# Kernel tuning notes

Hardware: AMD Instinct MI355X
Metric: run time of the kernel (lower is better)

Reference implementation:

```python
import jax, jax.numpy as jnp
import numpy as np
from jax import lax

B, V, C, H, W = 2, 8, 64, 128, 128
A = 256
C3 = 3 * C + 2  # 194 input channels for refine/confidence branches
CO = 3 * C      # 192 output channels of branch_refine
GROUPS = 8      # _group_count(192, 8) == 8
HID = max(4, CO // 4)  # 48 hidden channels in ChannelGate2d


def _conv3(x, w, b):
    y = lax.conv_general_dilated(x, w, (1, 1), 'SAME',
                                 dimension_numbers=('NCHW', 'OIHW', 'NCHW'))
    return y + b[None, :, None, None]


def _group_norm(x, scale, bias, groups, eps=1e-5):
    b, c, h, w = x.shape
    xg = x.reshape(b, groups, c // groups, h, w)
    mu = xg.mean(axis=(2, 3, 4), keepdims=True)
    var = xg.var(axis=(2, 3, 4), keepdims=True)
    xn = ((xg - mu) / jnp.sqrt(var + eps)).reshape(b, c, h, w)
    return xn * scale[None, :, None, None] + bias[None, :, None, None]


def _channel_gate(x, w1, b1, w2, b2):
    pooled = x.mean(axis=(2, 3))                     # [B,C]
    h = jax.nn.silu(pooled @ w1.T + b1)              # [B,HID]
    gate = jax.nn.sigmoid(h @ w2.T + b2)             # [B,C]
    return x * (0.5 + gate)[:, :, None, None]


def _conv_block(x, p):
    h = jax.nn.silu(_group_norm(_conv3(x, p['c1w'], p['c1b']), p['g1s'], p['g1b'], GROUPS))
    h = jax.nn.silu(_group_norm(_conv3(h, p['c2w'], p['c2b']), p['g2s'], p['g2b'], GROUPS))
    h = _channel_gate(h, p['gw1'], p['gb1'], p['gw2'], p['gb2'])
    res = jnp.einsum('bchw,oc->bohw', x, p['rpw']) + p['rpb'][None, :, None, None]
    return h + jnp.tanh(p['rs']) * res


def _fuse(vf, uvs, masks, importance, atlas_size):
    # vf:[B,V,C,H,W] uvs:[B,V,H,W,2] masks:[B,V,1,H,W] importance:[B,V]
    b, v, c, h, w = vf.shape
    P = atlas_size * atlas_size
    weights = jnp.maximum(importance.astype(vf.dtype), 0.0)
    finite = jnp.isfinite(uvs).all(axis=-1)                 # [B,V,H,W]
    valid = (masks[:, :, 0] > 0.5) & finite & (weights[:, :, None, None] > 0.0)
    safe = jnp.where(finite[..., None], uvs, 0.0)
    xi = jnp.round(jnp.clip(safe[..., 0], 0.0, 1.0) * (atlas_size - 1)).astype(jnp.int32)
    yi = jnp.round((1.0 - jnp.clip(safe[..., 1], 0.0, 1.0)) * (atlas_size - 1)).astype(jnp.int32)
    idx = (yi * atlas_size + xi).reshape(b, v * h * w)      # [B,N]
    wvalid = valid.astype(vf.dtype) * weights[:, :, None, None]
    feat = (vf * wvalid[:, :, None]).transpose(0, 2, 1, 3, 4).reshape(b, c, v * h * w)
    cnt = wvalid.reshape(b, v * h * w)

    def per_sample(f, cc, i):
        atlas = jax.ops.segment_sum(f.T, i, num_segments=P).T   # [C,P]
        counts = jax.ops.segment_sum(cc, i, num_segments=P)     # [P]
        return atlas, counts

    atlas, counts = jax.vmap(per_sample)(feat, cnt, idx)
    atlas = atlas.reshape(b, c, atlas_size, atlas_size)
    counts = counts.reshape(b, 1, atlas_size, atlas_size)
    fused = atlas / jnp.maximum(counts, 1.0)
    return fused, (counts > 0).astype(vf.dtype)


def _normalize_per_sample(t, eps=1e-6):
    scale = jnp.maximum(t.reshape(t.shape[0], -1).max(axis=1), eps)
    return jnp.clip(t / scale[:, None, None, None], 0.0, 1.0)


def setup_inputs() -> dict:
    key = jax.random.key(0)
    ks = jax.random.split(key, 20)
    inp = {
        'encoded_views': jax.random.normal(ks[0], (B, V, C, H, W), jnp.float32),
        'view_uvs': jax.random.uniform(ks[1], (B, V, H, W, 2), jnp.float32),
        'view_masks': jax.random.uniform(ks[2], (B, V, 1, H, W), jnp.float32),
        'w_global': jax.random.uniform(ks[3], (B, V), jnp.float32),
        'w_boundary': jax.random.uniform(ks[4], (B, V), jnp.float32),
        'w_highlight': jax.random.uniform(ks[5], (B, V), jnp.float32),
        'atlas_size': A,
        # ConvBlock params (random instead of zero-init so all paths are exercised)
        'c1w': jax.random.normal(ks[6], (CO, C3, 3, 3), jnp.float32) * 0.02,
        'c1b': jnp.zeros((CO,), jnp.float32),
        'g1s': jnp.ones((CO,), jnp.float32),
        'g1b': jnp.zeros((CO,), jnp.float32),
        'c2w': jax.random.normal(ks[7], (CO, CO, 3, 3), jnp.float32) * 0.02,
        'c2b': jnp.zeros((CO,), jnp.float32),
        'g2s': jnp.ones((CO,), jnp.float32),
        'g2b': jnp.zeros((CO,), jnp.float32),
        'gw1': jax.random.normal(ks[8], (HID, CO), jnp.float32) * 0.05,
        'gb1': jnp.zeros((HID,), jnp.float32),
        'gw2': jax.random.normal(ks[9], (CO, HID), jnp.float32) * 0.05,
        'gb2': jnp.zeros((CO,), jnp.float32),
        'rpw': jax.random.normal(ks[10], (CO, C3), jnp.float32) * 0.05,
        'rpb': jnp.zeros((CO,), jnp.float32),
        'rs': jnp.array(0.3, jnp.float32),
        'conf_w': jax.random.normal(ks[11], (3, C3), jnp.float32) * 0.05,
        'conf_b': jnp.zeros((3,), jnp.float32),
        'mix_scale': jnp.array(0.5, jnp.float32),
    }
    return inp


def reference(encoded_views, view_uvs, view_masks, w_global, w_boundary, w_highlight,
              atlas_size, c1w, c1b, g1s, g1b, c2w, c2b, g2s, g2b,
              gw1, gb1, gw2, gb2, rpw, rpb, rs, conf_w, conf_b, mix_scale):
    p = dict(c1w=c1w, c1b=c1b, g1s=g1s, g1b=g1b, c2w=c2w, c2b=c2b, g2s=g2s, g2b=g2b,
             gw1=gw1, gb1=gb1, gw2=gw2, gb2=gb2, rpw=rpw, rpb=rpb, rs=rs)
    g_feat, g_val = _fuse(encoded_views, view_uvs, view_masks, w_global, atlas_size)
    b_feat, b_val = _fuse(encoded_views, view_uvs, view_masks, w_boundary, atlas_size)
    h_feat, h_val = _fuse(encoded_views, view_uvs, view_masks, w_highlight, atlas_size)
    coverage = jnp.clip((g_val + b_val + h_val) / 3.0, 0.0, 1.0)
    stack = jnp.stack([g_feat, b_feat, h_feat], axis=1)     # [B,3,C,A,A]
    uncertainty = jnp.sqrt(stack.var(axis=1).mean(axis=1, keepdims=True))
    uncertainty = _normalize_per_sample(uncertainty) * coverage
    ctx = jnp.concatenate([g_feat, b_feat, h_feat, coverage, uncertainty], axis=1)
    refine = _conv_block(ctx, p)
    rg, rb, rh = jnp.split(refine, 3, axis=1)
    conf = jax.nn.sigmoid(jnp.einsum('bchw,oc->bohw', ctx, conf_w) + conf_b[None, :, None, None])
    ms = jnp.tanh(mix_scale)
    g_out = g_feat + ms * rg * conf[:, 0:1]
    b_out = b_feat + ms * rb * conf[:, 1:2]
    h_out = h_feat + ms * rh * conf[:, 2:3]
    return (g_out, b_out, h_out, coverage, uncertainty, conf)
```

## Files before the change

### kernel.cpp

```cpp
#include <hip/hip_runtime.h>
#include <math.h>

#define B_ 2
#define V_ 8
#define C_ 64
#define HW_ 16384
#define A_ 256
#define P_ 65536
#define CO_ 192
#define CPG_ 24
#define NG_ 8
#define ICP1 224
#define ICP2 192

#define OFF_ACC   0ull
#define SZ_ACC    (2ull*65536*192*4)
#define OFF_CNT   (OFF_ACC + SZ_ACC)
#define SZ_CNT    (2ull*3*65536*4)
#define OFF_CTXB  (OFF_CNT + SZ_CNT)
#define SZ_CTXB   (2ull*65536*224*2)
#define OFF_H1A   (OFF_CTXB + SZ_CTXB)
#define SZ_H1A    (2ull*65536*192*2)
#define OFF_W1    (OFF_H1A + SZ_H1A)
#define SZ_W1     (9ull*192*224*2)
#define OFF_W2    (OFF_W1 + SZ_W1)
#define SZ_W2     (9ull*192*192*2)
#define OFF_SM    (OFF_W2 + SZ_W2 + 256)

#define SM_STATS1 0
#define SM_STATS2 256
#define SM_SCALE  512
#define SM_POOLED 1024
#define SM_GATE   2560
#define SM_RAWU   8192

#define OUT_B    8388608
#define OUT_COV  25165824
#define OUT_UNC  25296896
#define OUT_CONF 25427968

typedef __attribute__((ext_vector_type(4))) float f32x4;
typedef __attribute__((ext_vector_type(8))) short bf16x8;

__device__ __forceinline__ float sigmoidf_(float x){ return 1.f/(1.f+expf(-x)); }
__device__ __forceinline__ float bf2f(unsigned short h){ return __uint_as_float(((unsigned)h)<<16); }
__device__ __forceinline__ unsigned short f2bf(float f){
  unsigned u = __float_as_uint(f);
  return (unsigned short)((u + 0x7fffu + ((u>>16)&1u)) >> 16);
}

__device__ __forceinline__ void gl_lds16(const void* g, void* l){
  __builtin_amdgcn_global_load_lds((const __attribute__((address_space(1))) void*)g,
                                   (__attribute__((address_space(3))) void*)l, 16, 0, 0);
}

__global__ __launch_bounds__(256) void k_prep(const float* __restrict__ c1w,
    const float* __restrict__ c2w, unsigned short* __restrict__ w1p, unsigned short* __restrict__ w2p)
{
  int idx = blockIdx.x*256 + threadIdx.x;
  const int N1 = 9*192*224;
  if (idx < N1){
    int ic = idx % 224; int oc = (idx/224) % 192; int k = idx/(224*192);
    float v = (ic < 194) ? c1w[(size_t)(oc*194+ic)*9 + k] : 0.f;
    w1p[idx] = f2bf(v);
  } else {
    int i2 = idx - N1;
    if (i2 < 9*192*192){
      int ic = i2 % 192; int oc = (i2/192) % 192; int k = i2/(192*192);
      w2p[i2] = f2bf(c2w[(size_t)(oc*192+ic)*9 + k]);
    }
  }
}

__global__ __launch_bounds__(256) void k_fuse(const float* __restrict__ vf,
    const float* __restrict__ uvs, const float* __restrict__ masks,
    const float* __restrict__ wgp, const float* __restrict__ wbp, const float* __restrict__ whp,
    float* __restrict__ acc, float* __restrict__ cnt)
{
  __shared__ __align__(16) float sf[64*65];
  __shared__ int sidx[64];
  __shared__ int svalid[64];
  __shared__ float sw[3];
  int t = threadIdx.x;
  int pix0 = blockIdx.x*64;
  int b   = pix0 / (V_*HW_);
  int rem = pix0 % (V_*HW_);
  int v   = rem / HW_;
  int p2  = rem % HW_;
  size_t vbase = ((size_t)(b*V_+v))*C_*HW_;
  for (int i=0;i<16;i++){
    int f = t + i*256;
    int c = f>>6, px = f&63;
    sf[c*65+px] = vf[vbase + (size_t)c*HW_ + p2 + px];
  }
  if (t<64){
    const float* u2 = uvs + (((size_t)(b*V_+v))*HW_ + p2 + t)*2;
    float ux = u2[0], uy = u2[1];
    int fin = isfinite(ux) && isfinite(uy);
    float su = fin?ux:0.f, svv = fin?uy:0.f;
    float cu = fminf(fmaxf(su,0.f),1.f);
    float cv = fminf(fmaxf(svv,0.f),1.f);
    int xi = (int)rintf(cu*255.f);
    int yi = (int)rintf((1.f-cv)*255.f);
    sidx[t] = yi*256+xi;
    float m = masks[((size_t)(b*V_+v))*HW_ + p2 + t];
    svalid[t] = (m>0.5f) && fin;
  }
  if (t<3){
    const float* wp = (t==0)?wgp:((t==1)?wbp:whp);
    sw[t] = fmaxf(wp[b*V_+v], 0.f);
  }
  __syncthreads();
  int wave = t>>6, lane = t&63;
  float w0 = sw[0], w1 = sw[1], w2 = sw[2];
  for (int i=0;i<16;i++){
    int px = wave*16+i;
    if (!svalid[px]) continue;
    int bin = sidx[px];
    float val = sf[lane*65+px];
    size_t base = ((size_t)b*P_ + bin)*192;
    if (w0>0.f) atomicAdd(&acc[base + lane],        val*w0);
    if (w1>0.f) atomicAdd(&acc[base + 64 + lane],   val*w1);
    if (w2>0.f) atomicAdd(&acc[base + 128 + lane],  val*w2);
    if (lane<3){
      float wv = sw[lane];
      if (wv>0.f) atomicAdd(&cnt[((size_t)(b*3+lane))*P_ + bin], wv);
    }
  }
}

__global__ __launch_bounds__(256) void k_finalize(const float* __restrict__ acc,
      const float* __restrict__ cnt, unsigned short* __restrict__ ctxb,
      float* __restrict__ out_cov, float* __restrict__ raw_unc, int* __restrict__ scale)
{
  __shared__ __align__(16) float sv[64*193];
  __shared__ float sc[3][64];
  __shared__ float up[256];
  __shared__ float s_cov[64];
  __shared__ float s_unc[64];
  int t = threadIdx.x;
  int bin0 = blockIdx.x*64;
  int b = bin0 >> 16;
  int p0 = bin0 & 65535;
  size_t abase = ((size_t)b*P_ + p0)*192;
  for (int i=0;i<48;i++){
    int f = t + i*256;
    int bl = f/192, c = f - bl*192;
    sv[bl*193+c] = acc[abase + f];
  }
  if (t<192){
    int br = t>>6, bl = t&63;
    sc[br][bl] = cnt[((size_t)(b*3+br))*P_ + p0 + bl];
  }
  __syncthreads();
  {
    int bl = t>>2, q = t&3;
    float dg = 1.f/fmaxf(sc[0][bl],1.f);
    float db = 1.f/fmaxf(sc[1][bl],1.f);
    float dh = 1.f/fmaxf(sc[2][bl],1.f);
    float s = 0.f;
    for (int j=0;j<16;j++){
      int c = q*16+j;
      float fg = sv[bl*193+c]*dg;
      float fb = sv[bl*193+64+c]*db;
      float fh = sv[bl*193+128+c]*dh;
      sv[bl*193+c]=fg; sv[bl*193+64+c]=fb; sv[bl*193+128+c]=fh;
      float m = (fg+fb+fh)*(1.f/3.f);
      float d0=fg-m, d1=fb-m, d2=fh-m;
      s += d0*d0+d1*d1+d2*d2;
    }
    up[t] = s;
  }
  __syncthreads();
  if (t<64){
    float tot = up[t*4]+up[t*4+1]+up[t*4+2]+up[t*4+3];
    float u = sqrtf(tot*(1.f/192.f));
    float vg = sc[0][t]>0.f?1.f:0.f;
    float vb = sc[1][t]>0.f?1.f:0.f;
    float vh = sc[2][t]>0.f?1.f:0.f;
    float cov = fminf(fmaxf((vg+vb+vh)*(1.f/3.f),0.f),1.f);
    s_cov[t] = cov; s_unc[t] = u;
    out_cov[(size_t)b*P_ + p0 + t] = cov;
    raw_unc[(size_t)b*P_ + p0 + t] = u;
    atomicMax(&scale[b], __float_as_int(u));
  }
  __syncthreads();
  for (int f=t; f<1792; f+=256){
    int cg = f % 28, bl = f / 28;
    int c0 = cg*8;
    unsigned short h[8];
    #pragma unroll
    for (int j=0;j<8;j++){
      int c = c0+j;
      float vv;
      if (c < 192)      vv = sv[bl*193+c];
      else if (c==192)  vv = s_cov[bl];
      else if (c==193)  vv = s_unc[bl];
      else              vv = 0.f;
      h[j] = f2bf(vv);
    }
    *(uint4*)&ctxb[((size_t)b*P_ + p0 + bl)*ICP1 + c0] = *(uint4*)h;
  }
}

__global__ __launch_bounds__(256) void k_norm_unc(unsigned short* __restrict__ ctxb,
    const int* __restrict__ scale, const float* __restrict__ raw_unc,
    const float* __restrict__ out_cov, float* __restrict__ out_unc)
{
  int tid = blockIdx.x*256 + threadIdx.x;
  int b = tid >> 16;
  float s = fmaxf(__int_as_float(scale[b]), 1e-6f);
  float u = raw_unc[tid];
  float cov = out_cov[tid];
  float un = fminf(fmaxf(u/s,0.f),1.f)*cov;
  out_unc[tid] = un;
  ctxb[(size_t)tid*ICP1 + 193] = f2bf(un);
}

template<int ICP, int CHUNKS>
__global__ __launch_bounds__(256,2) void k_conv3(const unsigned short* __restrict__ X,
    const unsigned short* __restrict__ Wp, const float* __restrict__ bias, float* __restrict__ Y,
    double* __restrict__ stats)
{
  __shared__ short s_in[2][258*32];
  __shared__ short s_w[576*32];
  __shared__ float sred[2][64];
  __shared__ float gsm[16];
  int t = threadIdx.x;
  int f_ = blockIdx.x + 128*(blockIdx.y + 3*blockIdx.z);
  int xcd = f_ & 7; int g_ = f_ >> 3;
  int ypair = xcd*16 + (g_ & 15);
  int h_  = g_ >> 4;
  int b   = h_ & 1;
  int oc0 = (h_ >> 1)*64;
  int y0  = ypair*2;
  int wv = t>>6, lane = t&63, l15 = lane&15, quad = lane>>4;

  f32x4 accA[4][4], accB[4][4];
  #pragma unroll
  for (int mt=0;mt<4;mt++){
    float4 bv = *(const float4*)&bias[oc0 + mt*16 + quad*4];
    f32x4 iv; iv.x=bv.x; iv.y=bv.y; iv.z=bv.z; iv.w=bv.w;
    #pragma unroll
    for (int nt=0;nt<4;nt++){ accA[mt][nt]=iv; accB[mt][nt]=iv; }
  }

  const unsigned short* Xb = X + (size_t)b*P_*ICP;

  if (t < 128){
    int bufi = t>>6, j = t&63;
    int idx = (j<32) ? j : (257*32 + (j-32));
    s_in[bufi][idx] = 0;
  }
  if (t < 128) sred[t>>6][t&63] = 0.f;
  if (t < 16)  gsm[t] = 0.f;

  auto issue_input = [&](int c2, int j2){
    int gy = y0 - 1 + j2;
    gy = min(max(gy,0),255);
    const unsigned short* src = Xb + ((size_t)gy*256)*ICP + c2*32;
    short* dst = &s_in[j2&1][0];
    #pragma unroll
    for (int i=0;i<4;i++){
      int f = t + i*256;
      int xi = 1 + (f>>2), icq = f&3;
      int icg = icq ^ ((xi>>1)&3);
      gl_lds16(src + (size_t)(xi-1)*ICP + icg*8, dst + 32 + (size_t)f*8);
    }
  };
  auto issue_wa = [&](int c2){
    int ic0n = c2*32;
    #pragma unroll
    for (int i=0;i<6;i++){
      int f = t + i*256;
      int oc = (f>>2)&63, icq = f&3;
      int r = i*64 + oc;
      int icg = icq ^ ((r>>1)&3);
      gl_lds16(Wp + ((size_t)(i*192) + oc0 + oc)*ICP + ic0n + icg*8, &s_w[(size_t)f*8]);
    }
  };
  auto issue_wb = [&](int c2){
    int ic0n = c2*32;
    #pragma unroll
    for (int i=0;i<3;i++){
      int f = t + i*256;
      int oc = (f>>2)&63, icq = f&3;
      int r = (6+i)*64 + oc;
      int icg = icq ^ ((r>>1)&3);
      gl_lds16(Wp + ((size_t)((6+i)*192) + oc0 + oc)*ICP + ic0n + icg*8, &s_w[(size_t)(1536+f)*8]);
    }
  };

  issue_wa(0);
  issue_input(0,0);
  issue_wb(0);
  issue_input(0,1);
  asm volatile("s_waitcnt lgkmcnt(0)" ::: "memory");

  for (int c=0; c<CHUNKS; ++c){
    #pragma unroll
    for (int j=0;j<4;++j){
      if (j==0)      asm volatile("s_waitcnt vmcnt(7)" ::: "memory");
      else if (j==1) asm volatile("s_waitcnt vmcnt(4)" ::: "memory");
      else if (j==2) asm volatile("s_waitcnt vmcnt(4)" ::: "memory");
      else {
        if (c==CHUNKS-1) asm volatile("s_waitcnt vmcnt(0)"  ::: "memory");
        else             asm volatile("s_waitcnt vmcnt(10)" ::: "memory");
      }
      __builtin_amdgcn_s_barrier();
      __builtin_amdgcn_sched_barrier(0);

      bool doA = (j<=2) && (y0 + j >= 1);
      bool doB = (j>=1) && (y0 - 1 + j <= 255);
      const short* si = &s_in[j&1][0];
      if (doA || doB){
        #pragma unroll
        for (int kx=0;kx<3;kx++){
          bf16x8 Bf[4];
          #pragma unroll
          for (int nt=0;nt<4;nt++){
            int r = wv*64 + nt*16 + l15 + kx;
            Bf[nt] = *(const bf16x8*)&si[r*32 + ((quad ^ ((r>>1)&3)))*8];
          }
          if (doA){
            bf16x8 Af[4];
            #pragma unroll
            for (int mt=0;mt<4;mt++){
              int r = j*192 + kx*64 + mt*16 + l15;
              Af[mt] = *(const bf16x8*)&s_w[r*32 + ((quad ^ ((r>>1)&3)))*8];
            }
            #pragma unroll
            for (int mt=0;mt<4;mt++)
              #pragma unroll
              for (int nt=0;nt<4;nt++)
                accA[mt][nt] = __builtin_amdgcn_mfma_f32_16x16x32_bf16(Af[mt], Bf[nt], accA[mt][nt], 0, 0, 0);
          }
          if (doB){
            bf16x8 Af[4];
            #pragma unroll
            for (int mt=0;mt<4;mt++){
              int r = (j-1)*192 + kx*64 + mt*16 + l15;
              Af[mt] = *(const bf16x8*)&s_w[r*32 + ((quad ^ ((r>>1)&3)))*8];
            }
            #pragma unroll
            for (int mt=0;mt<4;mt++)
              #pragma unroll
              for (int nt=0;nt<4;nt++)
                accB[mt][nt] = __builtin_amdgcn_mfma_f32_16x16x32_bf16(Af[mt], Bf[nt], accB[mt][nt], 0, 0, 0);
          }
        }
      }
      __builtin_amdgcn_s_barrier();
      __builtin_amdgcn_sched_barrier(0);
      if (j==2 && c+1<CHUNKS) issue_wa(c+1);
      if (j==3 && c+1<CHUNKS) issue_wb(c+1);
      if (!(c==CHUNKS-1 && j>=2))
        issue_input(j>=2 ? c+1 : c, (j+2)&3);
    }
  }

  float* Yb = Y + (size_t)b*P_*192;
  #pragma unroll
  for (int mt=0;mt<4;mt++){
    int oc = oc0 + mt*16 + quad*4;
    #pragma unroll
    for (int nt=0;nt<4;nt++){
      int px = wv*64 + nt*16 + l15;
      *(f32x4*)&Yb[(size_t)(y0*256+px)*192 + oc]     = accA[mt][nt];
      *(f32x4*)&Yb[(size_t)((y0+1)*256+px)*192 + oc] = accB[mt][nt];
    }
  }

  #pragma unroll
  for (int mt=0;mt<4;mt++)
    #pragma unroll
    for (int jj=0;jj<4;jj++){
      float v1 = accA[mt][0][jj]+accA[mt][1][jj]+accA[mt][2][jj]+accA[mt][3][jj]
               + accB[mt][0][jj]+accB[mt][1][jj]+accB[mt][2][jj]+accB[mt][3][jj];
      float v2 = accA[mt][0][jj]*accA[mt][0][jj]+accA[mt][1][jj]*accA[mt][1][jj]
               + accA[mt][2][jj]*accA[mt][2][jj]+accA[mt][3][jj]*accA[mt][3][jj]
               + accB[mt][0][jj]*accB[mt][0][jj]+accB[mt][1][jj]*accB[mt][1][jj]
               + accB[mt][2][jj]*accB[mt][2][jj]+accB[mt][3][jj]*accB[mt][3][jj];
      v1 += __shfl_xor(v1,1); v1 += __shfl_xor(v1,2); v1 += __shfl_xor(v1,4); v1 += __shfl_xor(v1,8);
      v2 += __shfl_xor(v2,1); v2 += __shfl_xor(v2,2); v2 += __shfl_xor(v2,4); v2 += __shfl_xor(v2,8);
      if (l15==0){
        int ocl = mt*16 + quad*4 + jj;
        atomicAdd(&sred[0][ocl], v1);
        atomicAdd(&sred[1][ocl], v2);
      }
    }
  __syncthreads();
  if (t < 64){
    int g = (oc0 + t)/24;
    atomicAdd(&gsm[g*2],   sred[0][t]);
    atomicAdd(&gsm[g*2+1], sred[1][t]);
  }
  __syncthreads();
  if (t < 8){
    int glo = oc0/24, ghi = (oc0+63)/24;
    if (t >= glo && t <= ghi){
      atomicAdd(&stats[(b*8+t)*2],   (double)gsm[t*2]);
      atomicAdd(&stats[(b*8+t)*2+1], (double)gsm[t*2+1]);
    }
  }
}

__global__ __launch_bounds__(256) void k_gn1_apply(const float* __restrict__ x, const double* __restrict__ stats,
    const float* __restrict__ gs, const float* __restrict__ gb, unsigned short* __restrict__ y)
{
  size_t i8 = ((size_t)blockIdx.x*256 + threadIdx.x)*8;
  int b = (int)(i8 / ((size_t)192*P_));
  int c = (int)(i8 % 192);
  int bg = b*8 + c/24;
  const double N = 24.0*65536.0;
  double mu = stats[bg*2]/N;
  double var = stats[bg*2+1]/N - mu*mu;
  float rstd = 1.0f/sqrtf((float)var + 1e-5f);
  float mean = (float)mu;
  float4 sA = *(const float4*)&gs[c];
  float4 sB = *(const float4*)&gs[c+4];
  float4 bA = *(const float4*)&gb[c];
  float4 bB = *(const float4*)&gb[c+4];
  float4 v0 = *(const float4*)&x[i8];
  float4 v1 = *(const float4*)&x[i8+4];
  float xin[8] = {v0.x,v0.y,v0.z,v0.w,v1.x,v1.y,v1.z,v1.w};
  float scl[8] = {sA.x,sA.y,sA.z,sA.w,sB.x,sB.y,sB.z,sB.w};
  float bia[8] = {bA.x,bA.y,bA.z,bA.w,bB.x,bB.y,bB.z,bB.w};
  unsigned short h[8];
  #pragma unroll
  for (int i=0;i<8;i++){
    float xn = (xin[i]-mean)*rstd*scl[i] + bia[i];
    h[i] = f2bf(xn*sigmoidf_(xn));
  }
  *(uint4*)&y[i8] = *(uint4*)h;
}

__global__ __launch_bounds__(256) void k_gn2_apply(float* __restrict__ x, const double* __restrict__ stats,
    const float* __restrict__ gs, const float* __restrict__ gb, float* __restrict__ pooled)
{
  __shared__ float pl[384];
  int t = threadIdx.x;
  for (int f=t; f<384; f+=256) pl[f]=0.f;
  int tid = blockIdx.x*256 + t;
  int c = (tid*8) % 192;
  float4 sA = *(const float4*)&gs[c];
  float4 sB = *(const float4*)&gs[c+4];
  float4 bA = *(const float4*)&gb[c];
  float4 bB = *(const float4*)&gb[c+4];
  float scl[8] = {sA.x,sA.y,sA.z,sA.w,sB.x,sB.y,sB.z,sB.w};
  float bia[8] = {bA.x,bA.y,bA.z,bA.w,bB.x,bB.y,bB.z,bB.w};
  float mean[2], rstd[2];
  #pragma unroll
  for (int bb=0;bb<2;bb++){
    int bg = bb*8 + c/24;
    const double N = 24.0*65536.0;
    double mu = stats[bg*2]/N;
    double var = stats[bg*2+1]/N - mu*mu;
    rstd[bb] = 1.0f/sqrtf((float)var + 1e-5f);
    mean[bb] = (float)mu;
  }
  float pacc[2][8] = {{0.f}};
  __syncthreads();
  #pragma unroll
  for (int k=0;k<8;k++){
    size_t i8 = ((size_t)tid + (size_t)k*393216)*8;
    int bb = k>>2;
    float4 v0 = *(const float4*)&x[i8];
    float4 v1 = *(const float4*)&x[i8+4];
    float xin[8] = {v0.x,v0.y,v0.z,v0.w,v1.x,v1.y,v1.z,v1.w};
    #pragma unroll
    for (int i=0;i<8;i++){
      float xn = (xin[i]-mean[bb])*rstd[bb]*scl[i] + bia[i];
      xn = xn*sigmoidf_(xn);
      xin[i] = xn;
      pacc[bb][i] += xn;
    }
    *(float4*)&x[i8]   = make_float4(xin[0],xin[1],xin[2],xin[3]);
    *(float4*)&x[i8+4] = make_float4(xin[4],xin[5],xin[6],xin[7]);
  }
  #pragma unroll
  for (int bb=0;bb<2;bb++)
    #pragma unroll
    for (int i=0;i<8;i++) atomicAdd(&pl[bb*192 + c + i], pacc[bb][i]);
  __syncthreads();
  for (int f=t; f<384; f+=256) atomicAdd(&pooled[f], pl[f]*(1.f/65536.f));
}

__global__ void k_gate(const float* __restrict__ pooled, const float* __restrict__ gw1,
    const float* __restrict__ gb1, const float* __restrict__ gw2, const float* __restrict__ gb2,
    float* __restrict__ gatef)
{
  __shared__ float hb[2*48];
  int t = threadIdx.x;
  if (t<96){
    int b=t/48, j=t%48;
    float a = gb1[j];
    for (int c=0;c<192;c++) a = fmaf(pooled[b*192+c], gw1[j*192+c], a);
    hb[t] = a*sigmoidf_(a);
  }
  __syncthreads();
  for (int i=t;i<384;i+=256){
    int b=i/192, c=i%192;
    float a = gb2[c];
    for (int j=0;j<48;j++) a = fmaf(hb[b*48+j], gw2[c*48+j], a);
    gatef[i] = 0.5f + sigmoidf_(a);
  }
}

__global__ __launch_bounds__(256) void k_conf(const unsigned short* __restrict__ ctxb,
    const float* __restrict__ cw, const float* __restrict__ cbias, float* __restrict__ out_conf)
{
  __shared__ float scw[3*224];
  int t = threadIdx.x;
  for (int f=t; f<672; f+=256){
    int c = f % 224, o = f / 224;
    scw[f] = (c<194) ? cw[o*194 + c] : 0.f;
  }
  __syncthreads();
  int tid = blockIdx.x*256 + t;
  int b = tid >> 16, p = tid & 65535;
  const unsigned short* cp = ctxb + ((size_t)b*P_ + p)*ICP1;
  float a0 = cbias[0], a1 = cbias[1], a2 = cbias[2];
  for (int q=0;q<28;q++){
    uint4 v = *(const uint4*)&cp[q*8];
    unsigned wd[4] = {v.x,v.y,v.z,v.w};
    #pragma unroll
    for (int j=0;j<8;j++){
      unsigned bits = wd[j>>1];
      float xf = (j&1) ? __uint_as_float(bits & 0xffff0000u) : __uint_as_float(bits<<16);
      int c = q*8+j;
      a0 = fmaf(xf, scw[c],       a0);
      a1 = fmaf(xf, scw[224+c],   a1);
      a2 = fmaf(xf, scw[448+c],   a2);
    }
  }
  out_conf[((size_t)(b*3+0))*P_ + p] = sigmoidf_(a0);
  out_conf[((size_t)(b*3+1))*P_ + p] = sigmoidf_(a1);
  out_conf[((size_t)(b*3+2))*P_ + p] = sigmoidf_(a2);
}

__global__ __launch_bounds__(256,4) void k_combine(const unsigned short* __restrict__ ctxb,
    const float* __restrict__ h2, const float* __restrict__ rpw, const float* __restrict__ rpb,
    const float* __restrict__ gatef, const float* __restrict__ conf_out,
    const float* __restrict__ rs, const float* __restrict__ mix, float* __restrict__ dout)
{
  __shared__ short s_x[256*32];
  __shared__ short s_w[64*32];
  int t = threadIdx.x;
  size_t p0 = (size_t)blockIdx.x*256;
  int oc0 = blockIdx.y*64, br = blockIdx.y;
  int wv = t>>6, lane = t&63, l15 = lane&15, quad = lane>>4;
  f32x4 acc[4][4];
  #pragma unroll
  for (int mt=0;mt<4;mt++){
    float4 bv = *(const float4*)&rpb[oc0 + mt*16 + quad*4];
    f32x4 iv; iv.x=bv.x; iv.y=bv.y; iv.z=bv.z; iv.w=bv.w;
    #pragma unroll
    for (int nt=0;nt<4;nt++) acc[mt][nt]=iv;
  }
  for (int ch=0; ch<7; ch++){
    int ic0 = ch*32;
    __syncthreads();
    for (int f=t; f<1024; f+=256){
      int icq = f&3, px = f>>2;
      uint4 v = *(const uint4*)&ctxb[(p0+px)*ICP1 + ic0 + icq*8];
      *(uint4*)&s_x[px*32 + ((icq ^ ((px>>1)&3)))*8] = v;
    }
    {
      int oc = t&63, icq = t>>6;
      unsigned short h[8];
      #pragma unroll
      for (int j=0;j<8;j++){
        int ic = ic0 + icq*8 + j;
        h[j] = (ic<194) ? f2bf(rpw[(size_t)(oc0+oc)*194 + ic]) : (unsigned short)0;
      }
      *(uint4*)&s_w[oc*32 + ((icq ^ ((oc>>1)&3)))*8] = *(uint4*)h;
    }
    __syncthreads();
    bf16x8 Af[4], Bf[4];
    #pragma unroll
    for (int mt=0;mt<4;mt++){
      int r = mt*16 + l15;
      Af[mt] = *(const bf16x8*)&s_w[r*32 + (((quad ^ ((r>>1)&3)))&3)*8];
    }
    #pragma unroll
    for (int nt=0;nt<4;nt++){
      int r = wv*64 + nt*16 + l15;
      Bf[nt] = *(const bf16x8*)&s_x[r*32 + (((quad ^ ((r>>1)&3)))&3)*8];
    }
    #pragma unroll
    for (int mt=0;mt<4;mt++)
      #pragma unroll
      for (int nt=0;nt<4;nt++)
        acc[mt][nt] = __builtin_amdgcn_mfma_f32_16x16x32_bf16(Af[mt], Bf[nt], acc[mt][nt], 0, 0, 0);
  }
  float trs = tanhf(rs[0]);
  float ms2 = tanhf(mix[0]);
  int b = (int)(p0 >> 16);
  #pragma unroll
  for (int mt=0;mt<4;mt++){
    int oc = oc0 + mt*16 + quad*4;
    int cc = oc & 63;
    float4 gv = *(const float4*)&gatef[b*192 + oc];
    #pragma unroll
    for (int nt=0;nt<4;nt++){
      size_t pf = p0 + wv*64 + nt*16 + l15;
      int p = (int)(pf & 65535);
      ushort4 fh = *(const ushort4*)&ctxb[pf*ICP1 + oc];
      float4 hv = *(const float4*)&h2[pf*192 + oc];
      float cf = conf_out[((size_t)(b*3+br))*P_ + p];
      size_t dst = (size_t)br*OUT_B + ((size_t)(b*64+cc))*P_ + p;
      dout[dst]            = bf2f(fh.x) + ms2*(hv.x*gv.x + trs*acc[mt][nt].x)*cf;
      dout[dst + P_]       = bf2f(fh.y) + ms2*(hv.y*gv.y + trs*acc[mt][nt].y)*cf;
      dout[dst + 2*P_]     = bf2f(fh.z) + ms2*(hv.z*gv.z + trs*acc[mt][nt].z)*cf;
      dout[dst + 3*P_]     = bf2f(fh.w) + ms2*(hv.w*gv.w + trs*acc[mt][nt].w)*cf;
    }
  }
}

extern "C" void kernel_launch(void* const* d_in, const int* in_sizes, int n_in,
                              void* d_out, int out_size, void* d_ws, size_t ws_size,
                              hipStream_t stream)
{
  const float* vf    = (const float*)d_in[0];
  const float* uvs   = (const float*)d_in[1];
  const float* masks = (const float*)d_in[2];
  const float* wg    = (const float*)d_in[3];
  const float* wb    = (const float*)d_in[4];
  const float* wh    = (const float*)d_in[5];
  const float* c1w = (const float*)d_in[7];
  const float* c1b = (const float*)d_in[8];
  const float* g1s = (const float*)d_in[9];
  const float* g1b = (const float*)d_in[10];
  const float* c2w = (const float*)d_in[11];
  const float* c2b = (const float*)d_in[12];
  const float* g2s = (const float*)d_in[13];
  const float* g2b = (const float*)d_in[14];
  const float* gw1 = (const float*)d_in[15];
  const float* gb1 = (const float*)d_in[16];
  const float* gw2 = (const float*)d_in[17];
  const float* gb2 = (const float*)d_in[18];
  const float* rpw = (const float*)d_in[19];
  const float* rpb = (const float*)d_in[20];
  const float* rs  = (const float*)d_in[21];
  const float* cw  = (const float*)d_in[22];
  const float* cb  = (const float*)d_in[23];
  const float* mix = (const float*)d_in[24];

  char* ws = (char*)d_ws;
  float*          accb  = (float*)(ws + OFF_ACC);
  float*          cntb  = (float*)(ws + OFF_CNT);
  unsigned short* ctxb  = (unsigned short*)(ws + OFF_CTXB);
  unsigned short* h1act = (unsigned short*)(ws + OFF_H1A);
  unsigned short* w1p   = (unsigned short*)(ws + OFF_W1);
  unsigned short* w2p   = (unsigned short*)(ws + OFF_W2);
  float*  h1raw  = (float*)(ws + OFF_ACC);
  float*  h2     = (float*)(ws + OFF_ACC);
  double* stats1 = (double*)(ws + OFF_SM + SM_STATS1);
  double* stats2 = (double*)(ws + OFF_SM + SM_STATS2);
  int*    scale  = (int*)(ws + OFF_SM + SM_SCALE);
  float*  pooled = (float*)(ws + OFF_SM + SM_POOLED);
  float*  gatef  = (float*)(ws + OFF_SM + SM_GATE);
  float*  rawu   = (float*)(ws + OFF_SM + SM_RAWU);

  float* out = (float*)d_out;
  float* out_cov  = out + OUT_COV;
  float* out_unc  = out + OUT_UNC;
  float* out_conf = out + OUT_CONF;

  hipMemsetAsync(ws + OFF_ACC, 0, SZ_ACC + SZ_CNT, stream);
  hipMemsetAsync(ws + OFF_SM, 0, 8192, stream);

  k_prep<<<2808, 256, 0, stream>>>(c1w, c2w, w1p, w2p);
  k_fuse<<<4096, 256, 0, stream>>>(vf, uvs, masks, wg, wb, wh, accb, cntb);
  k_finalize<<<2048, 256, 0, stream>>>(accb, cntb, ctxb, out_cov, rawu, scale);
  k_norm_unc<<<512, 256, 0, stream>>>(ctxb, scale, rawu, out_cov, out_unc);
  k_conv3<ICP1,7><<<dim3(128,3,2), 256, 0, stream>>>(ctxb, w1p, c1b, h1raw, stats1);
  k_gn1_apply<<<12288, 256, 0, stream>>>(h1raw, stats1, g1s, g1b, h1act);
  k_conv3<ICP2,6><<<dim3(128,3,2), 256, 0, stream>>>(h1act, w2p, c2b, h2, stats2);
  k_gn2_apply<<<1536, 256, 0, stream>>>(h2, stats2, g2s, g2b, pooled);
  k_gate<<<1, 256, 0, stream>>>(pooled, gw1, gb1, gw2, gb2, gatef);
  k_conf<<<512, 256, 0, stream>>>(ctxb, cw, cb, out_conf);
  k_combine<<<dim3(512,3), 256, 0, stream>>>(ctxb, h2, rpw, rpb, gatef, out_conf, rs, mix, out);
}
```

Measured before the change: 758.4 us.

## Store conv outputs in bf16, fold confidence head into finalize, vectorize fuse loads

The conv3 outputs (pre-norm h1 and h2) are now written as bf16 instead of fp32, which halves the traffic of the conv stores and of the group-norm and combine reads. The separate k_conf kernel is removed. Its dot product is computed in k_finalize from the fp32 accumulated features, and the uncertainty term plus sigmoid are finished in k_norm_unc. k_fuse now loads view features with float4 reads. The change lowers intermediate precision to bf16 before normalization and pooling, which may shift numerics slightly.

```diff
diff --git a/kernel.cpp b/kernel.cpp
--- a/kernel.cpp
+++ b/kernel.cpp
@@ -33,6 +33,7 @@
 #define SM_POOLED 1024
 #define SM_GATE   2560
 #define SM_RAWU   8192
+#define SM_CONFP  532480
 
 #define OUT_B    8388608
 #define OUT_COV  25165824
@@ -88,10 +89,12 @@
   int v   = rem / HW_;
   int p2  = rem % HW_;
   size_t vbase = ((size_t)(b*V_+v))*C_*HW_;
-  for (int i=0;i<16;i++){
+  for (int i=0;i<4;i++){
     int f = t + i*256;
-    int c = f>>6, px = f&63;
-    sf[c*65+px] = vf[vbase + (size_t)c*HW_ + p2 + px];
+    int c = f>>4, px4 = (f&15)*4;
+    float4 vv = *(const float4*)&vf[vbase + (size_t)c*HW_ + p2 + px4];
+    float* d = &sf[c*65+px4];
+    d[0]=vv.x; d[1]=vv.y; d[2]=vv.z; d[3]=vv.w;
   }
   if (t<64){
     const float* u2 = uvs + (((size_t)(b*V_+v))*HW_ + p2 + t)*2;
@@ -131,18 +134,22 @@
 
 __global__ __launch_bounds__(256) void k_finalize(const float* __restrict__ acc,
       const float* __restrict__ cnt, unsigned short* __restrict__ ctxb,
-      float* __restrict__ out_cov, float* __restrict__ raw_unc, int* __restrict__ scale)
+      float* __restrict__ out_cov, float* __restrict__ raw_unc, int* __restrict__ scale,
+      const float* __restrict__ cw, const float* __restrict__ cbias, float* __restrict__ confp)
 {
   __shared__ __align__(16) float sv[64*193];
   __shared__ float sc[3][64];
   __shared__ float up[256];
+  __shared__ float up3[3][256];
   __shared__ float s_cov[64];
   __shared__ float s_unc[64];
+  __shared__ float scw[582];
   int t = threadIdx.x;
   int bin0 = blockIdx.x*64;
   int b = bin0 >> 16;
   int p0 = bin0 & 65535;
   size_t abase = ((size_t)b*P_ + p0)*192;
+  for (int f=t; f<582; f+=256) scw[f] = cw[f];
   for (int i=0;i<48;i++){
     int f = t + i*256;
     int bl = f/192, c = f - bl*192;
@@ -185,6 +192,30 @@
     atomicMax(&scale[b], __float_as_int(u));
   }
   __syncthreads();
+  {
+    int bl = t>>2, q = t&3;
+    float q0=0.f,q1=0.f,q2=0.f;
+    for (int j=0;j<16;j++){
+      int c = q*16+j;
+      float fg = sv[bl*193+c];
+      float fb = sv[bl*193+64+c];
+      float fh = sv[bl*193+128+c];
+      q0 += fg*scw[c]     + fb*scw[64+c]     + fh*scw[128+c];
+      q1 += fg*scw[194+c] + fb*scw[258+c]    + fh*scw[322+c];
+      q2 += fg*scw[388+c] + fb*scw[452+c]    + fh*scw[516+c];
+    }
+    up3[0][t]=q0; up3[1][t]=q1; up3[2][t]=q2;
+  }
+  __syncthreads();
+  if (t<64){
+    float cov = s_cov[t];
+    #pragma unroll
+    for (int o=0;o<3;o++){
+      float pdot = up3[o][t*4]+up3[o][t*4+1]+up3[o][t*4+2]+up3[o][t*4+3]
+                 + cov*scw[o*194+192] + cbias[o];
+      confp[((size_t)(b*3+o))*P_ + p0 + t] = pdot;
+    }
+  }
   for (int f=t; f<1792; f+=256){
     int cg = f % 28, bl = f / 28;
     int c0 = cg*8;
@@ -205,21 +236,26 @@
 
 __global__ __launch_bounds__(256) void k_norm_unc(unsigned short* __restrict__ ctxb,
     const int* __restrict__ scale, const float* __restrict__ raw_unc,
-    const float* __restrict__ out_cov, float* __restrict__ out_unc)
+    const float* __restrict__ out_cov, float* __restrict__ out_unc,
+    const float* __restrict__ confp, const float* __restrict__ cw, float* __restrict__ out_conf)
 {
   int tid = blockIdx.x*256 + threadIdx.x;
-  int b = tid >> 16;
+  int b = tid >> 16, p = tid & 65535;
   float s = fmaxf(__int_as_float(scale[b]), 1e-6f);
   float u = raw_unc[tid];
   float cov = out_cov[tid];
   float un = fminf(fmaxf(u/s,0.f),1.f)*cov;
   out_unc[tid] = un;
   ctxb[(size_t)tid*ICP1 + 193] = f2bf(un);
+  float w0 = cw[193], w1 = cw[387], w2 = cw[581];
+  out_conf[((size_t)(b*3+0))*P_ + p] = sigmoidf_(confp[((size_t)(b*3+0))*P_ + p] + w0*un);
+  out_conf[((size_t)(b*3+1))*P_ + p] = sigmoidf_(confp[((size_t)(b*3+1))*P_ + p] + w1*un);
+  out_conf[((size_t)(b*3+2))*P_ + p] = sigmoidf_(confp[((size_t)(b*3+2))*P_ + p] + w2*un);
 }
 
 template<int ICP, int CHUNKS>
 __global__ __launch_bounds__(256,2) void k_conv3(const unsigned short* __restrict__ X,
-    const unsigned short* __restrict__ Wp, const float* __restrict__ bias, float* __restrict__ Y,
+    const unsigned short* __restrict__ Wp, const float* __restrict__ bias, unsigned short* __restrict__ Y,
     double* __restrict__ stats)
 {
   __shared__ short s_in[2][258*32];
@@ -359,15 +395,19 @@
     }
   }
 
-  float* Yb = Y + (size_t)b*P_*192;
+  unsigned short* Yb = Y + (size_t)b*P_*192;
   #pragma unroll
   for (int mt=0;mt<4;mt++){
     int oc = oc0 + mt*16 + quad*4;
     #pragma unroll
     for (int nt=0;nt<4;nt++){
       int px = wv*64 + nt*16 + l15;
-      *(f32x4*)&Yb[(size_t)(y0*256+px)*192 + oc]     = accA[mt][nt];
-      *(f32x4*)&Yb[(size_t)((y0+1)*256+px)*192 + oc] = accB[mt][nt];
+      f32x4 a = accA[mt][nt];
+      ushort4 ha; ha.x=f2bf(a.x); ha.y=f2bf(a.y); ha.z=f2bf(a.z); ha.w=f2bf(a.w);
+      *(ushort4*)&Yb[(size_t)(y0*256+px)*192 + oc] = ha;
+      f32x4 bb = accB[mt][nt];
+      ushort4 hb; hb.x=f2bf(bb.x); hb.y=f2bf(bb.y); hb.z=f2bf(bb.z); hb.w=f2bf(bb.w);
+      *(ushort4*)&Yb[(size_t)((y0+1)*256+px)*192 + oc] = hb;
     }
   }
 
@@ -405,7 +445,7 @@
   }
 }
 
-__global__ __launch_bounds__(256) void k_gn1_apply(const float* __restrict__ x, const double* __restrict__ stats,
+__global__ __launch_bounds__(256) void k_gn1_apply(const unsigned short* __restrict__ x, const double* __restrict__ stats,
     const float* __restrict__ gs, const float* __restrict__ gb, unsigned short* __restrict__ y)
 {
   size_t i8 = ((size_t)blockIdx.x*256 + threadIdx.x)*8;
@@ -421,21 +461,22 @@
   float4 sB = *(const float4*)&gs[c+4];
   float4 bA = *(const float4*)&gb[c];
   float4 bB = *(const float4*)&gb[c+4];
-  float4 v0 = *(const float4*)&x[i8];
-  float4 v1 = *(const float4*)&x[i8+4];
-  float xin[8] = {v0.x,v0.y,v0.z,v0.w,v1.x,v1.y,v1.z,v1.w};
+  uint4 vv = *(const uint4*)&x[i8];
+  unsigned wd[4] = {vv.x,vv.y,vv.z,vv.w};
   float scl[8] = {sA.x,sA.y,sA.z,sA.w,sB.x,sB.y,sB.z,sB.w};
   float bia[8] = {bA.x,bA.y,bA.z,bA.w,bB.x,bB.y,bB.z,bB.w};
   unsigned short h[8];
   #pragma unroll
   for (int i=0;i<8;i++){
-    float xn = (xin[i]-mean)*rstd*scl[i] + bia[i];
+    unsigned bits = wd[i>>1];
+    float xi = (i&1) ? __uint_as_float(bits & 0xffff0000u) : __uint_as_float(bits<<16);
+    float xn = (xi-mean)*rstd*scl[i] + bia[i];
     h[i] = f2bf(xn*sigmoidf_(xn));
   }
   *(uint4*)&y[i8] = *(uint4*)h;
 }
 
-__global__ __launch_bounds__(256) void k_gn2_apply(float* __restrict__ x, const double* __restrict__ stats,
+__global__ __launch_bounds__(256) void k_gn2_apply(unsigned short* __restrict__ x, const double* __restrict__ stats,
     const float* __restrict__ gs, const float* __restrict__ gb, float* __restrict__ pooled)
 {
   __shared__ float pl[384];
@@ -465,18 +506,19 @@
   for (int k=0;k<8;k++){
     size_t i8 = ((size_t)tid + (size_t)k*393216)*8;
     int bb = k>>2;
-    float4 v0 = *(const float4*)&x[i8];
-    float4 v1 = *(const float4*)&x[i8+4];
-    float xin[8] = {v0.x,v0.y,v0.z,v0.w,v1.x,v1.y,v1.z,v1.w};
+    uint4 vv = *(const uint4*)&x[i8];
+    unsigned wd[4] = {vv.x,vv.y,vv.z,vv.w};
+    unsigned short h[8];
     #pragma unroll
     for (int i=0;i<8;i++){
-      float xn = (xin[i]-mean[bb])*rstd[bb]*scl[i] + bia[i];
+      unsigned bits = wd[i>>1];
+      float xi = (i&1) ? __uint_as_float(bits & 0xffff0000u) : __uint_as_float(bits<<16);
+      float xn = (xi-mean[bb])*rstd[bb]*scl[i] + bia[i];
       xn = xn*sigmoidf_(xn);
-      xin[i] = xn;
-      pacc[bb][i] += xn;
-    }
-    *(float4*)&x[i8]   = make_float4(xin[0],xin[1],xin[2],xin[3]);
-    *(float4*)&x[i8+4] = make_float4(xin[4],xin[5],xin[6],xin[7]);
+      h[i] = f2bf(xn);
+      pacc[bb][i] += bf2f(h[i]);
+    }
+    *(uint4*)&x[i8] = *(uint4*)h;
   }
   #pragma unroll
   for (int bb=0;bb<2;bb++)
@@ -507,40 +549,8 @@
   }
 }
 
-__global__ __launch_bounds__(256) void k_conf(const unsigned short* __restrict__ ctxb,
-    const float* __restrict__ cw, const float* __restrict__ cbias, float* __restrict__ out_conf)
-{
-  __shared__ float scw[3*224];
-  int t = threadIdx.x;
-  for (int f=t; f<672; f+=256){
-    int c = f % 224, o = f / 224;
-    scw[f] = (c<194) ? cw[o*194 + c] : 0.f;
-  }
-  __syncthreads();
-  int tid = blockIdx.x*256 + t;
-  int b = tid >> 16, p = tid & 65535;
-  const unsigned short* cp = ctxb + ((size_t)b*P_ + p)*ICP1;
-  float a0 = cbias[0], a1 = cbias[1], a2 = cbias[2];
-  for (int q=0;q<28;q++){
-    uint4 v = *(const uint4*)&cp[q*8];
-    unsigned wd[4] = {v.x,v.y,v.z,v.w};
-    #pragma unroll
-    for (int j=0;j<8;j++){
-      unsigned bits = wd[j>>1];
-      float xf = (j&1) ? __uint_as_float(bits & 0xffff0000u) : __uint_as_float(bits<<16);
-      int c = q*8+j;
-      a0 = fmaf(xf, scw[c],       a0);
-      a1 = fmaf(xf, scw[224+c],   a1);
-      a2 = fmaf(xf, scw[448+c],   a2);
-    }
-  }
-  out_conf[((size_t)(b*3+0))*P_ + p] = sigmoidf_(a0);
-  out_conf[((size_t)(b*3+1))*P_ + p] = sigmoidf_(a1);
-  out_conf[((size_t)(b*3+2))*P_ + p] = sigmoidf_(a2);
-}
-
 __global__ __launch_bounds__(256,4) void k_combine(const unsigned short* __restrict__ ctxb,
-    const float* __restrict__ h2, const float* __restrict__ rpw, const float* __restrict__ rpb,
+    const unsigned short* __restrict__ h2, const float* __restrict__ rpw, const float* __restrict__ rpb,
     const float* __restrict__ gatef, const float* __restrict__ conf_out,
     const float* __restrict__ rs, const float* __restrict__ mix, float* __restrict__ dout)
 {
@@ -607,13 +617,13 @@
       size_t pf = p0 + wv*64 + nt*16 + l15;
       int p = (int)(pf & 65535);
       ushort4 fh = *(const ushort4*)&ctxb[pf*ICP1 + oc];
-      float4 hv = *(const float4*)&h2[pf*192 + oc];
+      ushort4 hh = *(const ushort4*)&h2[pf*192 + oc];
       float cf = conf_out[((size_t)(b*3+br))*P_ + p];
       size_t dst = (size_t)br*OUT_B + ((size_t)(b*64+cc))*P_ + p;
-      dout[dst]            = bf2f(fh.x) + ms2*(hv.x*gv.x + trs*acc[mt][nt].x)*cf;
-      dout[dst + P_]       = bf2f(fh.y) + ms2*(hv.y*gv.y + trs*acc[mt][nt].y)*cf;
-      dout[dst + 2*P_]     = bf2f(fh.z) + ms2*(hv.z*gv.z + trs*acc[mt][nt].z)*cf;
-      dout[dst + 3*P_]     = bf2f(fh.w) + ms2*(hv.w*gv.w + trs*acc[mt][nt].w)*cf;
+      dout[dst]            = bf2f(fh.x) + ms2*(bf2f(hh.x)*gv.x + trs*acc[mt][nt].x)*cf;
+      dout[dst + P_]       = bf2f(fh.y) + ms2*(bf2f(hh.y)*gv.y + trs*acc[mt][nt].y)*cf;
+      dout[dst + 2*P_]     = bf2f(fh.z) + ms2*(bf2f(hh.z)*gv.z + trs*acc[mt][nt].z)*cf;
+      dout[dst + 3*P_]     = bf2f(fh.w) + ms2*(bf2f(hh.w)*gv.w + trs*acc[mt][nt].w)*cf;
     }
   }
 }
@@ -654,14 +664,15 @@
   unsigned short* h1act = (unsigned short*)(ws + OFF_H1A);
   unsigned short* w1p   = (unsigned short*)(ws + OFF_W1);
   unsigned short* w2p   = (unsigned short*)(ws + OFF_W2);
-  float*  h1raw  = (float*)(ws + OFF_ACC);
-  float*  h2     = (float*)(ws + OFF_ACC);
+  unsigned short* h1pre = (unsigned short*)(ws + OFF_ACC);
+  unsigned short* h2    = (unsigned short*)(ws + OFF_ACC);
   double* stats1 = (double*)(ws + OFF_SM + SM_STATS1);
   double* stats2 = (double*)(ws + OFF_SM + SM_STATS2);
   int*    scale  = (int*)(ws + OFF_SM + SM_SCALE);
   float*  pooled = (float*)(ws + OFF_SM + SM_POOLED);
   float*  gatef  = (float*)(ws + OFF_SM + SM_GATE);
   float*  rawu   = (float*)(ws + OFF_SM + SM_RAWU);
+  float*  confp  = (float*)(ws + OFF_SM + SM_CONFP);
 
   float* out = (float*)d_out;
   float* out_cov  = out + OUT_COV;
@@ -673,13 +684,12 @@
 
   k_prep<<<2808, 256, 0, stream>>>(c1w, c2w, w1p, w2p);
   k_fuse<<<4096, 256, 0, stream>>>(vf, uvs, masks, wg, wb, wh, accb, cntb);
-  k_finalize<<<2048, 256, 0, stream>>>(accb, cntb, ctxb, out_cov, rawu, scale);
-  k_norm_unc<<<512, 256, 0, stream>>>(ctxb, scale, rawu, out_cov, out_unc);
-  k_conv3<ICP1,7><<<dim3(128,3,2), 256, 0, stream>>>(ctxb, w1p, c1b, h1raw, stats1);
-  k_gn1_apply<<<12288, 256, 0, stream>>>(h1raw, stats1, g1s, g1b, h1act);
+  k_finalize<<<2048, 256, 0, stream>>>(accb, cntb, ctxb, out_cov, rawu, scale, cw, cb, confp);
+  k_norm_unc<<<512, 256, 0, stream>>>(ctxb, scale, rawu, out_cov, out_unc, confp, cw, out_conf);
+  k_conv3<ICP1,7><<<dim3(128,3,2), 256, 0, stream>>>(ctxb, w1p, c1b, h1pre, stats1);
+  k_gn1_apply<<<12288, 256, 0, stream>>>(h1pre, stats1, g1s, g1b, h1act);
   k_conv3<ICP2,6><<<dim3(128,3,2), 256, 0, stream>>>(h1act, w2p, c2b, h2, stats2);
   k_gn2_apply<<<1536, 256, 0, stream>>>(h2, stats2, g2s, g2b, pooled);
   k_gate<<<1, 256, 0, stream>>>(pooled, gw1, gb1, gw2, gb2, gatef);
-  k_conf<<<512, 256, 0, stream>>>(ctxb, cw, cb, out_conf);
   k_combine<<<dim3(512,3), 256, 0, stream>>>(ctxb, h2, rpw, rpb, gatef, out_conf, rs, mix, out);
 }
```

Result: faster. 718.4 us (-5.3%).
